# Kernel tuning notes

Measured on AMD Instinct MI355X. Metric: run time of the kernel, lower is better.

## Reference

```python
import jax, jax.numpy as jnp
import numpy as np

B, S, E = 2, 2048, 1024
H = 32
DK = E // H  # 32, must equal H for the bilinear einsum to type-check
FFN = 4096
EPS = 1e-5


def layer_norm(x, g, b):
    m = jnp.mean(x, axis=-1, keepdims=True)
    v = jnp.mean((x - m) ** 2, axis=-1, keepdims=True)
    return (x - m) * jax.lax.rsqrt(v + EPS) * g + b


def setup_inputs() -> dict:
    key = jax.random.key(0)
    ks = jax.random.split(key, 16)
    sc = lambda fan_in: 1.0 / np.sqrt(fan_in)
    return {
        "x": jax.random.normal(ks[0], (B, S, E), jnp.float32),
        "Wq": jax.random.normal(ks[1], (E, E), jnp.float32) * sc(E),
        "bq": jax.random.normal(ks[2], (E,), jnp.float32) * 0.02,
        "Wk": jax.random.normal(ks[3], (E, E), jnp.float32) * sc(E),
        "bk": jax.random.normal(ks[4], (E,), jnp.float32) * 0.02,
        "Wv": jax.random.normal(ks[5], (E, E), jnp.float32) * sc(E),
        "bv": jax.random.normal(ks[6], (E,), jnp.float32) * 0.02,
        "kernelW": jax.random.normal(ks[7], (DK, H), jnp.float32),
        "Wo": jax.random.normal(ks[8], (E, E), jnp.float32) * sc(E),
        "bo": jax.random.normal(ks[9], (E,), jnp.float32) * 0.02,
        "W1": jax.random.normal(ks[10], (E, FFN), jnp.float32) * sc(E),
        "b1": jax.random.normal(ks[11], (FFN,), jnp.float32) * 0.02,
        "W2": jax.random.normal(ks[12], (FFN, E), jnp.float32) * sc(FFN),
        "b2": jax.random.normal(ks[13], (E,), jnp.float32) * 0.02,
        "g1": jnp.ones((E,), jnp.float32),
        "beta1": jnp.zeros((E,), jnp.float32),
        "g2": jnp.ones((E,), jnp.float32),
        "beta2": jnp.zeros((E,), jnp.float32),
    }


def reference(x, Wq, bq, Wk, bk, Wv, bv, kernelW, Wo, bo, W1, b1, W2, b2, g1, beta1, g2, beta2):
    # projections -> [B, H, S, DK]
    split = lambda t: t.reshape(B, S, H, DK).transpose(0, 2, 1, 3)
    q = split(x @ Wq + bq)
    k = split(x @ Wk + bk)
    v = split(x @ Wv + bv)
    # bilinear quantum-kernel score: sim[b,h,i,j] = sum_d q[b,h,i,d]*W[d,h]*k[b,h,j,d]
    sim = jnp.einsum('bhqd,dh,bhkd->bhqk', q, kernelW, k)
    attn = jax.nn.softmax(sim, axis=-1)  # dropout is identity at eval
    out = jnp.matmul(attn, v)  # [B, H, S, DK]
    out = out.transpose(0, 2, 1, 3).reshape(B, S, E) @ Wo + bo
    x = layer_norm(x + out, g1, beta1)
    ffn = jax.nn.relu(x @ W1 + b1) @ W2 + b2
    return layer_norm(x + ffn, g2, beta2)
```

## Files before the change

kernel.cpp:

```cpp
#include <hip/hip_runtime.h>


typedef unsigned short u16;
typedef unsigned int u32;
typedef __bf16 bf16x8 __attribute__((ext_vector_type(8)));
typedef float f32x4 __attribute__((ext_vector_type(4)));
typedef float f32x16 __attribute__((ext_vector_type(16)));

__device__ __forceinline__ u16 f2b(float f) {
  union { float f; unsigned u; } x; x.f = f;
  unsigned r = x.u + 0x7FFFu + ((x.u >> 16) & 1u);
  return (u16)(r >> 16);
}

__device__ __forceinline__ float b2f(u16 u) {
  union { u32 u; float f; } x; x.u = (u32)u << 16; return x.f;
}

__device__ __forceinline__ unsigned pkbf(float lo, float hi) {
  unsigned r;
  asm("v_cvt_pk_bf16_f32 %0, %1, %2" : "=v"(r) : "v"(lo), "v"(hi));
  return r;
}

__device__ __forceinline__ float expo2(float x) {
#if __has_builtin(__builtin_amdgcn_exp2f)
  return __builtin_amdgcn_exp2f(x);
#else
  return exp2f(x);
#endif
}

#define GLDS16(gp, lp)                                                         \
  __builtin_amdgcn_global_load_lds(                                            \
      (const __attribute__((address_space(1))) void*)(gp),                     \
      (__attribute__((address_space(3))) void*)(lp), 16, 0, 0)

__global__ __launch_bounds__(256) void transpose_cast(
    const float* __restrict__ W, u16* __restrict__ WT, int K, int N) {
  __shared__ float tile[32][33];
  const int tx = threadIdx.x & 31, ty = threadIdx.x >> 5;
  const int n0 = blockIdx.x * 32, k0 = blockIdx.y * 32;
#pragma unroll
  for (int i = 0; i < 4; ++i)
    tile[ty + 8 * i][tx] = W[(size_t)(k0 + ty + 8 * i) * N + n0 + tx];
  __syncthreads();
#pragma unroll
  for (int i = 0; i < 4; ++i)
    WT[(size_t)(n0 + ty + 8 * i) * K + k0 + tx] = f2b(tile[tx][ty + 8 * i]);
}

__global__ __launch_bounds__(256) void cast_b(const float* __restrict__ x,
                                              u16* __restrict__ y) {
  int i = blockIdx.x * 256 + threadIdx.x;
  float4 v = ((const float4*)x)[i];
  ushort4 o;
  o.x = f2b(v.x); o.y = f2b(v.y); o.z = f2b(v.z); o.w = f2b(v.w);
  ((ushort4*)y)[i] = o;
}

template <int MODE, int BN>
__global__ __launch_bounds__(256) void gemmT(
    const u16* __restrict__ A, const u16* __restrict__ BT,
    const float* __restrict__ bias, const float* __restrict__ bias2,
    const float* __restrict__ bias3, const float* __restrict__ res,
    void* __restrict__ outp, const float* __restrict__ kW, int N_, int K_) {
  constexpr int ABYT = 128 * 32 * 2;
  constexpr int BBYT = BN * 32 * 2;
  constexpr int STRIDE = ABYT + BBYT;
  constexpr int MI = (BN == 128) ? 4 : 2;
  __shared__ __align__(16) char SH[2 * STRIDE];
  const int t = threadIdx.x, lane = t & 63, wid = t >> 6;
  const int gx = gridDim.x;
  const int id = blockIdx.y * gx + blockIdx.x;
  const int nb = gx * gridDim.y;
  const int sid = (id & 7) * (nb >> 3) + (id >> 3);
  const int bx = sid % gx;
  int by = sid / gx;
  int kh6 = 0;
  if constexpr (MODE == 6) { kh6 = by >> 5; by &= 31; }
  const int m0 = by * 128, n0 = bx * BN;
  const int wr = (BN == 128) ? (wid >> 1) * 64 : wid * 32;
  const int wc = (BN == 128) ? (wid & 1) * 64 : 0;
  const int lr = lane & 15, lg = lane >> 4;
  const int K = K_;
  const int koff = (MODE == 6) ? kh6 * 1024 : 0;

  f32x4 acc[MI][4] = {};

  const u16* ga0 = A + (size_t)(m0 + (t >> 2)) * K + koff + (t & 3) * 8;
  const u16* ga1 = ga0 + (size_t)64 * K;
  const u16* gb0 = BT + (size_t)(n0 + (t >> 2)) * K + koff + (t & 3) * 8;
  const u16* gb1 = gb0 + (size_t)64 * K;
  const int stA = wid * 1024;

#define STAGE(CUR, KT)                                                         \
  {                                                                            \
    char* l_ = (char*)SH + (CUR) * STRIDE + stA;                               \
    const size_t o_ = (size_t)(KT) * 32;                                       \
    GLDS16(ga0 + o_, l_);                                                      \
    GLDS16(ga1 + o_, l_ + 4096);                                               \
    GLDS16(gb0 + o_, l_ + ABYT);                                               \
    if constexpr (BN == 128) GLDS16(gb1 + o_, l_ + ABYT + 4096);               \
  }

  const int nk = (MODE == 6) ? 32 : (K >> 5);
  STAGE(0, 0);
  __syncthreads();
  int cur = 0;
  for (int kt = 0; kt < nk; ++kt) {
    if (kt + 1 < nk) STAGE(cur ^ 1, kt + 1);
    const char* l = (const char*)SH + cur * STRIDE;
    bf16x8 af[MI], bf[4];
#pragma unroll
    for (int i = 0; i < MI; ++i)
      af[i] = *(const bf16x8*)(l + (wr + i * 16 + lr) * 64 + lg * 16);
#pragma unroll
    for (int i = 0; i < 4; ++i)
      bf[i] = *(const bf16x8*)(l + ABYT + (wc + i * 16 + lr) * 64 + lg * 16);
#pragma unroll
    for (int mi = 0; mi < MI; ++mi)
#pragma unroll
      for (int ni = 0; ni < 4; ++ni)
        acc[mi][ni] = __builtin_amdgcn_mfma_f32_16x16x32_bf16(
            af[mi], bf[ni], acc[mi][ni], 0, 0, 0);
    __syncthreads();
    cur ^= 1;
  }
#undef STAGE

#pragma unroll
  for (int mi = 0; mi < MI; ++mi) {
#pragma unroll
    for (int ni = 0; ni < 4; ++ni) {
      const int row = m0 + wr + mi * 16 + lg * 4;
      const int col = n0 + wc + ni * 16 + lr;
      f32x4 v = acc[mi][ni];
      if constexpr (MODE == 2) {
        const float bv = bias[col];
        float* o = (float*)outp;
#pragma unroll
        for (int r = 0; r < 4; ++r) {
          const int rr = row + r;
          o[(size_t)rr * N_ + col] = v[r] + bv + res[(size_t)rr * N_ + col];
        }
      } else if constexpr (MODE == 3) {
        const float bv = bias[col];
        u16* o = (u16*)outp;
#pragma unroll
        for (int r = 0; r < 4; ++r) {
          const int rr = row + r;
          float y = v[r] + bv;
          o[(size_t)rr * N_ + col] = f2b(y > 0.f ? y : 0.f);
        }
      } else if constexpr (MODE == 6) {
        u16* o = (kh6 < 2) ? ((u16*)outp + (size_t)kh6 * 4194304)
                           : ((u16*)res + (size_t)(kh6 - 2) * 4194304);
#pragma unroll
        for (int r = 0; r < 4; ++r) {
          const int rr = row + r;
          o[(size_t)rr * N_ + col] = f2b(v[r]);
        }
      } else {
        const int proj = col >> 10, c = col & 1023;
        const int h = c >> 5, d = c & 31;
        u16* qout = (u16*)outp;
        if (proj == 0) {
          const float bv = bias[c];
          const float sc = kW[d * 32 + h] * 1.44269504089f;
#pragma unroll
          for (int r = 0; r < 4; ++r) {
            const int rr = row + r;
            const int bb = rr >> 11, s = rr & 2047;
            qout[(size_t)(((bb * 32 + h) * 2048) + s) * 32 + d] =
                f2b((v[r] + bv) * sc);
          }
        } else if (proj == 1) {
          const float bv = bias2[c];
          u16* kout = qout + 4194304;
          const int c2 = d >> 3;
#pragma unroll
          for (int r = 0; r < 4; ++r) {
            const int rr = row + r;
            const int bb = rr >> 11, s = rr & 2047;
            const int k = s & 63;
            const int g = ((k >> 5) << 1) | (c2 >> 1);
            kout[(size_t)(bb * 32 + h) * 65536 + (s >> 6) * 2048 + g * 512 +
                 (c2 & 1) * 256 + (k & 31) * 8 + (d & 7)] = f2b(v[r] + bv);
          }
        } else {
          const float bv = bias3[c];
          u16* vout = qout + 8388608;
          const int bb = row >> 11, s0 = row & 2047;
          const int k = s0 & 63;
          const int cc = k >> 3, rb = cc >> 1, hb = cc & 1, e = k & 7;
          ushort4 st;
          st.x = f2b(v[0] + bv); st.y = f2b(v[1] + bv);
          st.z = f2b(v[2] + bv); st.w = f2b(v[3] + bv);
          *(ushort4*)(vout + (size_t)(bb * 32 + h) * 65536 +
                      (s0 >> 6) * 2048 + rb * 512 + hb * 256 + d * 8 + e) = st;
        }
      }
    }
  }
}

__device__ __forceinline__ void attn_tile(
    const bf16x8& k0, const bf16x8& k1, const bf16x8& k2, const bf16x8& k3,
    const bf16x8& v0, const bf16x8& v1, const bf16x8& v2, const bf16x8& v3,
    const bf16x8& qb0, const bf16x8& qb1,
    f32x16& acc, float& la, float& lb, float& lc, float& ld) {
  const f32x16 z16 = {};
  f32x16 s0 = __builtin_amdgcn_mfma_f32_32x32x16_bf16(k0, qb0, z16, 0, 0, 0);
  s0 = __builtin_amdgcn_mfma_f32_32x32x16_bf16(k1, qb1, s0, 0, 0, 0);
  f32x16 s1 = __builtin_amdgcn_mfma_f32_32x32x16_bf16(k2, qb0, z16, 0, 0, 0);
  s1 = __builtin_amdgcn_mfma_f32_32x32x16_bf16(k3, qb1, s1, 0, 0, 0);
  float p0[16], p1[16];
#pragma unroll
  for (int r = 0; r < 16; ++r) p0[r] = expo2(s0[r]);
#pragma unroll
  for (int r = 0; r < 16; ++r) p1[r] = expo2(s1[r]);
#pragma unroll
  for (int r = 0; r < 4; ++r) {
    la += p0[r] + p1[r];
    lb += p0[4 + r] + p1[4 + r];
    lc += p0[8 + r] + p1[8 + r];
    ld += p0[12 + r] + p1[12 + r];
  }
  {
    u32 x0 = pkbf(p0[0], p0[1]), x1 = pkbf(p0[2], p0[3]);
    u32 y0 = pkbf(p0[4], p0[5]), y1 = pkbf(p0[6], p0[7]);
    asm("v_permlane32_swap_b32 %0, %1" : "+v"(x0), "+v"(y0));
    asm("v_permlane32_swap_b32 %0, %1" : "+v"(x1), "+v"(y1));
    union { u32 d[4]; bf16x8 v; } u;
    u.d[0] = x0; u.d[1] = x1; u.d[2] = y0; u.d[3] = y1;
    acc = __builtin_amdgcn_mfma_f32_32x32x16_bf16(v0, u.v, acc, 0, 0, 0);
  }
  {
    u32 x0 = pkbf(p0[8], p0[9]), x1 = pkbf(p0[10], p0[11]);
    u32 y0 = pkbf(p0[12], p0[13]), y1 = pkbf(p0[14], p0[15]);
    asm("v_permlane32_swap_b32 %0, %1" : "+v"(x0), "+v"(y0));
    asm("v_permlane32_swap_b32 %0, %1" : "+v"(x1), "+v"(y1));
    union { u32 d[4]; bf16x8 v; } u;
    u.d[0] = x0; u.d[1] = x1; u.d[2] = y0; u.d[3] = y1;
    acc = __builtin_amdgcn_mfma_f32_32x32x16_bf16(v1, u.v, acc, 0, 0, 0);
  }
  {
    u32 x0 = pkbf(p1[0], p1[1]), x1 = pkbf(p1[2], p1[3]);
    u32 y0 = pkbf(p1[4], p1[5]), y1 = pkbf(p1[6], p1[7]);
    asm("v_permlane32_swap_b32 %0, %1" : "+v"(x0), "+v"(y0));
    asm("v_permlane32_swap_b32 %0, %1" : "+v"(x1), "+v"(y1));
    union { u32 d[4]; bf16x8 v; } u;
    u.d[0] = x0; u.d[1] = x1; u.d[2] = y0; u.d[3] = y1;
    acc = __builtin_amdgcn_mfma_f32_32x32x16_bf16(v2, u.v, acc, 0, 0, 0);
  }
  {
    u32 x0 = pkbf(p1[8], p1[9]), x1 = pkbf(p1[10], p1[11]);
    u32 y0 = pkbf(p1[12], p1[13]), y1 = pkbf(p1[14], p1[15]);
    asm("v_permlane32_swap_b32 %0, %1" : "+v"(x0), "+v"(y0));
    asm("v_permlane32_swap_b32 %0, %1" : "+v"(x1), "+v"(y1));
    union { u32 d[4]; bf16x8 v; } u;
    u.d[0] = x0; u.d[1] = x1; u.d[2] = y0; u.d[3] = y1;
    acc = __builtin_amdgcn_mfma_f32_32x32x16_bf16(v3, u.v, acc, 0, 0, 0);
  }
}

__global__ __launch_bounds__(512) void attn_kernel(
    const u16* __restrict__ Q, const u16* __restrict__ K,
    const u16* __restrict__ VT, u16* __restrict__ O) {
  __shared__ __align__(16) char LDSB[32768];
  const int t = threadIdx.x, wid = t >> 6, lane = t & 63;
  const int qg = wid & 3, kh = wid >> 2;
  const int bid = blockIdx.x;
  const int swz = (bid & 7) * 128 + (bid >> 3);
  const int bh = swz >> 4;
  const int qt = swz & 15;
  const int q0 = qt * 128 + qg * 32;
  const int lq = lane & 31, hi = lane >> 5;
  const u16* Qh = Q + (size_t)bh * 65536;
  const u16* Kh = K + (size_t)bh * 65536;
  const u16* Vh = VT + (size_t)bh * 65536;

  const bf16x8 qb0 = *(const bf16x8*)(Qh + (size_t)(q0 + lq) * 32 + hi * 8);
  const bf16x8 qb1 = *(const bf16x8*)(Qh + (size_t)(q0 + lq) * 32 + 16 + hi * 8);

  const u16* kg = Kh + wid * 512 + lane * 8;
  const u16* vg = Vh + wid * 512 + lane * 8;
  const int lds_w = wid * 1024;

#define STAGEA(CUR, I)                                                         \
  if (wid < 4) {                                                               \
    char* b_ = LDSB + (CUR) * 16384 + lds_w;                                   \
    GLDS16(kg + (size_t)(I) * 2048, b_);                                       \
    GLDS16(vg + (size_t)(I) * 2048, b_ + 4096);                                \
    GLDS16(kg + (size_t)(16 + (I)) * 2048, b_ + 8192);                         \
    GLDS16(vg + (size_t)(16 + (I)) * 2048, b_ + 12288);                        \
  }

  f32x16 acc = {};
  float la = 0.f, lb = 0.f, lc = 0.f, ld = 0.f;

  STAGEA(0, 0);
  __syncthreads();
  int cur = 0;
#pragma unroll 1
  for (int i = 0; i < 16; ++i) {
    if (i < 15) STAGEA(cur ^ 1, i + 1);
    const char* kb = LDSB + cur * 16384 + kh * 8192 + lane * 16;
    const bf16x8 ka0 = *(const bf16x8*)(kb);
    const bf16x8 ka1 = *(const bf16x8*)(kb + 1024);
    const bf16x8 ka2 = *(const bf16x8*)(kb + 2048);
    const bf16x8 ka3 = *(const bf16x8*)(kb + 3072);
    const bf16x8 va0 = *(const bf16x8*)(kb + 4096);
    const bf16x8 va1 = *(const bf16x8*)(kb + 5120);
    const bf16x8 va2 = *(const bf16x8*)(kb + 6144);
    const bf16x8 va3 = *(const bf16x8*)(kb + 7168);
    attn_tile(ka0, ka1, ka2, ka3, va0, va1, va2, va3, qb0, qb1,
              acc, la, lb, lc, ld);
    __syncthreads();
    cur ^= 1;
  }
#undef STAGEA

  float lrun = (la + lb) + (lc + ld);
  lrun += __shfl_xor(lrun, 32);

  float* sm_acc = (float*)LDSB;
  float* sm_l = (float*)(LDSB + 16384);
  if (kh == 1) {
    sm_l[qg * 32 + lq] = lrun;
#pragma unroll
    for (int r = 0; r < 16; ++r) sm_acc[(qg * 64 + lane) * 16 + r] = acc[r];
  }
  __syncthreads();
  if (kh == 0) {
    const float inv = 1.f / (lrun + sm_l[qg * 32 + lq]);
    const int bb = bh >> 5, h = bh & 31;
    u16* o = O + (size_t)(bb * 2048 + q0 + lq) * 1024 + h * 32;
#pragma unroll
    for (int g = 0; g < 4; ++g) {
      ushort4 st;
      st.x = f2b((acc[g * 4 + 0] + sm_acc[(qg * 64 + lane) * 16 + g * 4 + 0]) * inv);
      st.y = f2b((acc[g * 4 + 1] + sm_acc[(qg * 64 + lane) * 16 + g * 4 + 1]) * inv);
      st.z = f2b((acc[g * 4 + 2] + sm_acc[(qg * 64 + lane) * 16 + g * 4 + 2]) * inv);
      st.w = f2b((acc[g * 4 + 3] + sm_acc[(qg * 64 + lane) * 16 + g * 4 + 3]) * inv);
      *(ushort4*)(o + g * 8 + hi * 4) = st;
    }
  }
}

template <int WB>
__global__ __launch_bounds__(256) void ln_kernel(
    const float* X, const float* __restrict__ g, const float* __restrict__ b,
    float* outf, u16* __restrict__ outb) {
  const int wid = threadIdx.x >> 6, lane = threadIdx.x & 63;
  const int row = blockIdx.x * 4 + wid;
  const float4* X4 = (const float4*)(X + (size_t)row * 1024);
  float4 xs[4];
  float s = 0.f, sq = 0.f;
#pragma unroll
  for (int i = 0; i < 4; ++i) {
    xs[i] = X4[lane + i * 64];
    s += xs[i].x + xs[i].y + xs[i].z + xs[i].w;
    sq += xs[i].x * xs[i].x + xs[i].y * xs[i].y + xs[i].z * xs[i].z + xs[i].w * xs[i].w;
  }
#pragma unroll
  for (int m = 1; m < 64; m <<= 1) { s += __shfl_xor(s, m); sq += __shfl_xor(sq, m); }
  const float mean = s * (1.f / 1024.f);
  float var = sq * (1.f / 1024.f) - mean * mean;
  var = var > 0.f ? var : 0.f;
  const float rstd = rsqrtf(var + 1e-5f);
  const float4* g4 = (const float4*)g;
  const float4* b4 = (const float4*)b;
  float4* of = (float4*)(outf + (size_t)row * 1024);
#pragma unroll
  for (int i = 0; i < 4; ++i) {
    const int c = lane + i * 64;
    const float4 gv = g4[c], bv = b4[c], x = xs[i];
    float4 y;
    y.x = (x.x - mean) * rstd * gv.x + bv.x;
    y.y = (x.y - mean) * rstd * gv.y + bv.y;
    y.z = (x.z - mean) * rstd * gv.z + bv.z;
    y.w = (x.w - mean) * rstd * gv.w + bv.w;
    of[c] = y;
    if constexpr (WB) {
      ushort4 yb;
      yb.x = f2b(y.x); yb.y = f2b(y.y); yb.z = f2b(y.z); yb.w = f2b(y.w);
      ((ushort4*)(outb + (size_t)row * 1024))[c] = yb;
    }
  }
}

__global__ __launch_bounds__(256) void ln2sum_kernel(
    const u16* __restrict__ P0, const u16* __restrict__ P1,
    const u16* __restrict__ P2, const u16* __restrict__ P3,
    const float* __restrict__ R, const float* __restrict__ bias,
    const float* __restrict__ g, const float* __restrict__ b,
    float* __restrict__ out) {
  const int wid = threadIdx.x >> 6, lane = threadIdx.x & 63;
  const int row = blockIdx.x * 4 + wid;
  const ushort4* A4 = (const ushort4*)(P0 + (size_t)row * 1024);
  const ushort4* B4 = (const ushort4*)(P1 + (size_t)row * 1024);
  const ushort4* C4 = (const ushort4*)(P2 + (size_t)row * 1024);
  const ushort4* D4 = (const ushort4*)(P3 + (size_t)row * 1024);
  const float4* R4 = (const float4*)(R + (size_t)row * 1024);
  const float4* Bi4 = (const float4*)bias;
  float4 xs[4];
  float s = 0.f, sq = 0.f;
#pragma unroll
  for (int i = 0; i < 4; ++i) {
    const int c = lane + i * 64;
    const ushort4 a = A4[c], pb = B4[c], pc = C4[c], pd = D4[c];
    const float4 r = R4[c], bi = Bi4[c];
    float4 x;
    x.x = (b2f(a.x) + b2f(pb.x)) + (b2f(pc.x) + b2f(pd.x)) + r.x + bi.x;
    x.y = (b2f(a.y) + b2f(pb.y)) + (b2f(pc.y) + b2f(pd.y)) + r.y + bi.y;
    x.z = (b2f(a.z) + b2f(pb.z)) + (b2f(pc.z) + b2f(pd.z)) + r.z + bi.z;
    x.w = (b2f(a.w) + b2f(pb.w)) + (b2f(pc.w) + b2f(pd.w)) + r.w + bi.w;
    xs[i] = x;
    s += x.x + x.y + x.z + x.w;
    sq += x.x * x.x + x.y * x.y + x.z * x.z + x.w * x.w;
  }
#pragma unroll
  for (int m = 1; m < 64; m <<= 1) { s += __shfl_xor(s, m); sq += __shfl_xor(sq, m); }
  const float mean = s * (1.f / 1024.f);
  float var = sq * (1.f / 1024.f) - mean * mean;
  var = var > 0.f ? var : 0.f;
  const float rstd = rsqrtf(var + 1e-5f);
  const float4* g4 = (const float4*)g;
  const float4* b4 = (const float4*)b;
  float4* of = (float4*)(out + (size_t)row * 1024);
#pragma unroll
  for (int i = 0; i < 4; ++i) {
    const int c = lane + i * 64;
    const float4 gv = g4[c], bv = b4[c], x = xs[i];
    float4 y;
    y.x = (x.x - mean) * rstd * gv.x + bv.x;
    y.y = (x.y - mean) * rstd * gv.y + bv.y;
    y.z = (x.z - mean) * rstd * gv.z + bv.z;
    y.w = (x.w - mean) * rstd * gv.w + bv.w;
    of[c] = y;
  }
}

extern "C" void kernel_launch(void* const* d_in, const int* in_sizes, int n_in,
                              void* d_out, int out_size, void* d_ws,
                              size_t ws_size, hipStream_t stream) {
  const float* x   = (const float*)d_in[0];
  const float* Wq  = (const float*)d_in[1];
  const float* bq  = (const float*)d_in[2];
  const float* Wk  = (const float*)d_in[3];
  const float* bk  = (const float*)d_in[4];
  const float* Wv  = (const float*)d_in[5];
  const float* bv  = (const float*)d_in[6];
  const float* kW  = (const float*)d_in[7];
  const float* Wo  = (const float*)d_in[8];
  const float* bo  = (const float*)d_in[9];
  const float* W1  = (const float*)d_in[10];
  const float* b1  = (const float*)d_in[11];
  const float* W2  = (const float*)d_in[12];
  const float* b2  = (const float*)d_in[13];
  const float* g1  = (const float*)d_in[14];
  const float* be1 = (const float*)d_in[15];
  const float* g2  = (const float*)d_in[16];
  const float* be2 = (const float*)d_in[17];

  char* ws = (char*)d_ws;
  const size_t MB = 1024 * 1024;
  u16*   WqT = (u16*)(ws + 0 * MB);
  u16*   WoT = (u16*)(ws + 6 * MB);
  u16*   W1T = (u16*)(ws + 8 * MB);
  u16*   W2T = (u16*)(ws + 16 * MB);
  float* r1  = (float*)(ws + 24 * MB);
  u16*   xb  = (u16*)(ws + 40 * MB);
  u16*   qhB = (u16*)(ws + 48 * MB);
  u16*   khB = (u16*)(ws + 56 * MB);
  u16*   vTB = (u16*)(ws + 64 * MB);
  u16*   hf  = (u16*)(ws + 40 * MB);
  u16*   ao  = (u16*)(ws + 72 * MB);
  u16*   x1b = (u16*)(ws + 80 * MB);
  u16*   p0  = (u16*)(ws + 0 * MB);
  u16*   p2  = (u16*)(ws + 72 * MB);

  const dim3 blk(256);

  transpose_cast<<<dim3(32, 32), blk, 0, stream>>>(Wq, WqT, 1024, 1024);
  transpose_cast<<<dim3(32, 32), blk, 0, stream>>>(Wk, WqT + 1048576, 1024, 1024);
  transpose_cast<<<dim3(32, 32), blk, 0, stream>>>(Wv, WqT + 2097152, 1024, 1024);
  transpose_cast<<<dim3(32, 32), blk, 0, stream>>>(Wo, WoT, 1024, 1024);
  transpose_cast<<<dim3(128, 32), blk, 0, stream>>>(W1, W1T, 1024, 4096);
  transpose_cast<<<dim3(32, 128), blk, 0, stream>>>(W2, W2T, 4096, 1024);
  cast_b<<<4096, blk, 0, stream>>>(x, xb);

  gemmT<5, 128><<<dim3(24, 32), blk, 0, stream>>>(
      xb, WqT, bq, bk, bv, nullptr, qhB, kW, 3072, 1024);

  attn_kernel<<<1024, dim3(512), 0, stream>>>(qhB, khB, vTB, ao);

  gemmT<2, 64><<<dim3(16, 32), blk, 0, stream>>>(
      ao, WoT, bo, nullptr, nullptr, x, r1, nullptr, 1024, 1024);
  ln_kernel<1><<<1024, blk, 0, stream>>>(r1, g1, be1, r1, x1b);
  gemmT<3, 128><<<dim3(32, 32), blk, 0, stream>>>(
      x1b, W1T, b1, nullptr, nullptr, nullptr, hf, nullptr, 4096, 1024);
  gemmT<6, 128><<<dim3(8, 128), blk, 0, stream>>>(
      hf, W2T, nullptr, nullptr, nullptr, (const float*)p2, p0, nullptr,
      1024, 4096);
  ln2sum_kernel<<<1024, blk, 0, stream>>>(p0, p0 + 4194304, p2, p2 + 4194304,
                                          r1, b2, g2, be2, (float*)d_out);

  (void)in_sizes; (void)n_in; (void)out_size; (void)ws_size;
}
```

Measured before the change: 253.5 us.

## Merge prep launches into one kernel and keep LN1 residual stream in bf16

Combines the six weight transpose-casts and the input cast into a single prep kernel indexed by block id, removing several launches. The attention output projection now reads the bf16 copy of x as residual and writes bf16; LayerNorm1 normalizes that buffer in place, and the final sum reads it as bf16. This cuts fp32 traffic and drops a separate buffer, at the cost of reduced precision in the residual path.

```diff
diff --git a/kernel.cpp b/kernel.cpp
--- a/kernel.cpp
+++ b/kernel.cpp
@@ -36,27 +36,47 @@
       (const __attribute__((address_space(1))) void*)(gp),                     \
       (__attribute__((address_space(3))) void*)(lp), 16, 0, 0)
 
-__global__ __launch_bounds__(256) void transpose_cast(
-    const float* __restrict__ W, u16* __restrict__ WT, int K, int N) {
+__global__ __launch_bounds__(256) void prep_kernel(
+    const float* __restrict__ Wq, const float* __restrict__ Wk,
+    const float* __restrict__ Wv, const float* __restrict__ Wo,
+    const float* __restrict__ W1, const float* __restrict__ W2,
+    const float* __restrict__ x, u16* __restrict__ WqT, u16* __restrict__ WoT,
+    u16* __restrict__ W1T, u16* __restrict__ W2T, u16* __restrict__ xb) {
   __shared__ float tile[32][33];
-  const int tx = threadIdx.x & 31, ty = threadIdx.x >> 5;
-  const int n0 = blockIdx.x * 32, k0 = blockIdx.y * 32;
-#pragma unroll
-  for (int i = 0; i < 4; ++i)
-    tile[ty + 8 * i][tx] = W[(size_t)(k0 + ty + 8 * i) * N + n0 + tx];
-  __syncthreads();
-#pragma unroll
-  for (int i = 0; i < 4; ++i)
-    WT[(size_t)(n0 + ty + 8 * i) * K + k0 + tx] = f2b(tile[tx][ty + 8 * i]);
-}
-
-__global__ __launch_bounds__(256) void cast_b(const float* __restrict__ x,
-                                              u16* __restrict__ y) {
-  int i = blockIdx.x * 256 + threadIdx.x;
-  float4 v = ((const float4*)x)[i];
-  ushort4 o;
-  o.x = f2b(v.x); o.y = f2b(v.y); o.z = f2b(v.z); o.w = f2b(v.w);
-  ((ushort4*)y)[i] = o;
+  const int id = blockIdx.x;
+  if (id < 12288) {
+    const float* W; u16* WT; int K, N, bx, by;
+    if (id < 4096) {
+      const int w = id >> 10, local = id & 1023;
+      bx = local & 31; by = local >> 5; K = 1024; N = 1024;
+      W = (w == 0) ? Wq : (w == 1) ? Wk : (w == 2) ? Wv : Wo;
+      WT = (w == 0) ? WqT : (w == 1) ? WqT + 1048576
+           : (w == 2) ? WqT + 2097152 : WoT;
+    } else if (id < 8192) {
+      const int local = id - 4096;
+      bx = local & 127; by = local >> 7; K = 1024; N = 4096;
+      W = W1; WT = W1T;
+    } else {
+      const int local = id - 8192;
+      bx = local & 31; by = local >> 5; K = 4096; N = 1024;
+      W = W2; WT = W2T;
+    }
+    const int tx = threadIdx.x & 31, ty = threadIdx.x >> 5;
+    const int n0 = bx * 32, k0 = by * 32;
+#pragma unroll
+    for (int i = 0; i < 4; ++i)
+      tile[ty + 8 * i][tx] = W[(size_t)(k0 + ty + 8 * i) * N + n0 + tx];
+    __syncthreads();
+#pragma unroll
+    for (int i = 0; i < 4; ++i)
+      WT[(size_t)(n0 + ty + 8 * i) * K + k0 + tx] = f2b(tile[tx][ty + 8 * i]);
+  } else {
+    const int i = (id - 12288) * 256 + threadIdx.x;
+    float4 v = ((const float4*)x)[i];
+    ushort4 o;
+    o.x = f2b(v.x); o.y = f2b(v.y); o.z = f2b(v.z); o.w = f2b(v.w);
+    ((ushort4*)xb)[i] = o;
+  }
 }
 
 template <int MODE, int BN>
@@ -138,11 +158,13 @@
       f32x4 v = acc[mi][ni];
       if constexpr (MODE == 2) {
         const float bv = bias[col];
-        float* o = (float*)outp;
+        u16* o = (u16*)outp;
+        const u16* rb = (const u16*)res;
 #pragma unroll
         for (int r = 0; r < 4; ++r) {
           const int rr = row + r;
-          o[(size_t)rr * N_ + col] = v[r] + bv + res[(size_t)rr * N_ + col];
+          o[(size_t)rr * N_ + col] =
+              f2b(v[r] + bv + b2f(rb[(size_t)rr * N_ + col]));
         }
       } else if constexpr (MODE == 3) {
         const float bv = bias[col];
@@ -349,20 +371,22 @@
   }
 }
 
-template <int WB>
-__global__ __launch_bounds__(256) void ln_kernel(
-    const float* X, const float* __restrict__ g, const float* __restrict__ b,
-    float* outf, u16* __restrict__ outb) {
+__global__ __launch_bounds__(256) void ln1b_kernel(
+    u16* __restrict__ X, const float* __restrict__ g,
+    const float* __restrict__ b) {
   const int wid = threadIdx.x >> 6, lane = threadIdx.x & 63;
   const int row = blockIdx.x * 4 + wid;
-  const float4* X4 = (const float4*)(X + (size_t)row * 1024);
+  ushort4* X4 = (ushort4*)(X + (size_t)row * 1024);
   float4 xs[4];
   float s = 0.f, sq = 0.f;
 #pragma unroll
   for (int i = 0; i < 4; ++i) {
-    xs[i] = X4[lane + i * 64];
-    s += xs[i].x + xs[i].y + xs[i].z + xs[i].w;
-    sq += xs[i].x * xs[i].x + xs[i].y * xs[i].y + xs[i].z * xs[i].z + xs[i].w * xs[i].w;
+    const ushort4 u = X4[lane + i * 64];
+    float4 v;
+    v.x = b2f(u.x); v.y = b2f(u.y); v.z = b2f(u.z); v.w = b2f(u.w);
+    xs[i] = v;
+    s += v.x + v.y + v.z + v.w;
+    sq += v.x * v.x + v.y * v.y + v.z * v.z + v.w * v.w;
   }
 #pragma unroll
   for (int m = 1; m < 64; m <<= 1) { s += __shfl_xor(s, m); sq += __shfl_xor(sq, m); }
@@ -372,29 +396,23 @@
   const float rstd = rsqrtf(var + 1e-5f);
   const float4* g4 = (const float4*)g;
   const float4* b4 = (const float4*)b;
-  float4* of = (float4*)(outf + (size_t)row * 1024);
 #pragma unroll
   for (int i = 0; i < 4; ++i) {
     const int c = lane + i * 64;
     const float4 gv = g4[c], bv = b4[c], x = xs[i];
-    float4 y;
-    y.x = (x.x - mean) * rstd * gv.x + bv.x;
-    y.y = (x.y - mean) * rstd * gv.y + bv.y;
-    y.z = (x.z - mean) * rstd * gv.z + bv.z;
-    y.w = (x.w - mean) * rstd * gv.w + bv.w;
-    of[c] = y;
-    if constexpr (WB) {
-      ushort4 yb;
-      yb.x = f2b(y.x); yb.y = f2b(y.y); yb.z = f2b(y.z); yb.w = f2b(y.w);
-      ((ushort4*)(outb + (size_t)row * 1024))[c] = yb;
-    }
+    ushort4 yb;
+    yb.x = f2b((x.x - mean) * rstd * gv.x + bv.x);
+    yb.y = f2b((x.y - mean) * rstd * gv.y + bv.y);
+    yb.z = f2b((x.z - mean) * rstd * gv.z + bv.z);
+    yb.w = f2b((x.w - mean) * rstd * gv.w + bv.w);
+    X4[c] = yb;
   }
 }
 
 __global__ __launch_bounds__(256) void ln2sum_kernel(
     const u16* __restrict__ P0, const u16* __restrict__ P1,
     const u16* __restrict__ P2, const u16* __restrict__ P3,
-    const float* __restrict__ R, const float* __restrict__ bias,
+    const u16* __restrict__ R, const float* __restrict__ bias,
     const float* __restrict__ g, const float* __restrict__ b,
     float* __restrict__ out) {
   const int wid = threadIdx.x >> 6, lane = threadIdx.x & 63;
@@ -403,20 +421,20 @@
   const ushort4* B4 = (const ushort4*)(P1 + (size_t)row * 1024);
   const ushort4* C4 = (const ushort4*)(P2 + (size_t)row * 1024);
   const ushort4* D4 = (const ushort4*)(P3 + (size_t)row * 1024);
-  const float4* R4 = (const float4*)(R + (size_t)row * 1024);
+  const ushort4* R4 = (const ushort4*)(R + (size_t)row * 1024);
   const float4* Bi4 = (const float4*)bias;
   float4 xs[4];
   float s = 0.f, sq = 0.f;
 #pragma unroll
   for (int i = 0; i < 4; ++i) {
     const int c = lane + i * 64;
-    const ushort4 a = A4[c], pb = B4[c], pc = C4[c], pd = D4[c];
-    const float4 r = R4[c], bi = Bi4[c];
+    const ushort4 a = A4[c], pb = B4[c], pc = C4[c], pd = D4[c], rr = R4[c];
+    const float4 bi = Bi4[c];
     float4 x;
-    x.x = (b2f(a.x) + b2f(pb.x)) + (b2f(pc.x) + b2f(pd.x)) + r.x + bi.x;
-    x.y = (b2f(a.y) + b2f(pb.y)) + (b2f(pc.y) + b2f(pd.y)) + r.y + bi.y;
-    x.z = (b2f(a.z) + b2f(pb.z)) + (b2f(pc.z) + b2f(pd.z)) + r.z + bi.z;
-    x.w = (b2f(a.w) + b2f(pb.w)) + (b2f(pc.w) + b2f(pd.w)) + r.w + bi.w;
+    x.x = (b2f(a.x) + b2f(pb.x)) + (b2f(pc.x) + b2f(pd.x)) + b2f(rr.x) + bi.x;
+    x.y = (b2f(a.y) + b2f(pb.y)) + (b2f(pc.y) + b2f(pd.y)) + b2f(rr.y) + bi.y;
+    x.z = (b2f(a.z) + b2f(pb.z)) + (b2f(pc.z) + b2f(pd.z)) + b2f(rr.z) + bi.z;
+    x.w = (b2f(a.w) + b2f(pb.w)) + (b2f(pc.w) + b2f(pd.w)) + b2f(rr.w) + bi.w;
     xs[i] = x;
     s += x.x + x.y + x.z + x.w;
     sq += x.x * x.x + x.y * x.y + x.z * x.z + x.w * x.w;
@@ -471,26 +489,20 @@
   u16*   WoT = (u16*)(ws + 6 * MB);
   u16*   W1T = (u16*)(ws + 8 * MB);
   u16*   W2T = (u16*)(ws + 16 * MB);
-  float* r1  = (float*)(ws + 24 * MB);
+  u16*   r1b = (u16*)(ws + 24 * MB);
   u16*   xb  = (u16*)(ws + 40 * MB);
   u16*   qhB = (u16*)(ws + 48 * MB);
   u16*   khB = (u16*)(ws + 56 * MB);
   u16*   vTB = (u16*)(ws + 64 * MB);
   u16*   hf  = (u16*)(ws + 40 * MB);
   u16*   ao  = (u16*)(ws + 72 * MB);
-  u16*   x1b = (u16*)(ws + 80 * MB);
   u16*   p0  = (u16*)(ws + 0 * MB);
   u16*   p2  = (u16*)(ws + 72 * MB);
 
   const dim3 blk(256);
 
-  transpose_cast<<<dim3(32, 32), blk, 0, stream>>>(Wq, WqT, 1024, 1024);
-  transpose_cast<<<dim3(32, 32), blk, 0, stream>>>(Wk, WqT + 1048576, 1024, 1024);
-  transpose_cast<<<dim3(32, 32), blk, 0, stream>>>(Wv, WqT + 2097152, 1024, 1024);
-  transpose_cast<<<dim3(32, 32), blk, 0, stream>>>(Wo, WoT, 1024, 1024);
-  transpose_cast<<<dim3(128, 32), blk, 0, stream>>>(W1, W1T, 1024, 4096);
-  transpose_cast<<<dim3(32, 128), blk, 0, stream>>>(W2, W2T, 4096, 1024);
-  cast_b<<<4096, blk, 0, stream>>>(x, xb);
+  prep_kernel<<<16384, blk, 0, stream>>>(Wq, Wk, Wv, Wo, W1, W2, x,
+                                         WqT, WoT, W1T, W2T, xb);
 
   gemmT<5, 128><<<dim3(24, 32), blk, 0, stream>>>(
       xb, WqT, bq, bk, bv, nullptr, qhB, kW, 3072, 1024);
@@ -498,15 +510,16 @@
   attn_kernel<<<1024, dim3(512), 0, stream>>>(qhB, khB, vTB, ao);
 
   gemmT<2, 64><<<dim3(16, 32), blk, 0, stream>>>(
-      ao, WoT, bo, nullptr, nullptr, x, r1, nullptr, 1024, 1024);
-  ln_kernel<1><<<1024, blk, 0, stream>>>(r1, g1, be1, r1, x1b);
+      ao, WoT, bo, nullptr, nullptr, (const float*)xb, r1b, nullptr,
+      1024, 1024);
+  ln1b_kernel<<<1024, blk, 0, stream>>>(r1b, g1, be1);
   gemmT<3, 128><<<dim3(32, 32), blk, 0, stream>>>(
-      x1b, W1T, b1, nullptr, nullptr, nullptr, hf, nullptr, 4096, 1024);
+      r1b, W1T, b1, nullptr, nullptr, nullptr, hf, nullptr, 4096, 1024);
   gemmT<6, 128><<<dim3(8, 128), blk, 0, stream>>>(
       hf, W2T, nullptr, nullptr, nullptr, (const float*)p2, p0, nullptr,
       1024, 4096);
   ln2sum_kernel<<<1024, blk, 0, stream>>>(p0, p0 + 4194304, p2, p2 + 4194304,
-                                          r1, b2, g2, be2, (float*)d_out);
+                                          r1b, b2, g2, be2, (float*)d_out);
 
   (void)in_sizes; (void)n_in; (void)out_size; (void)ws_size;
 }
```

Result: faster. 235.9 us (-6.9%).
